# Optimization experiments

Measured on AMD Instinct MI355X. Metric: run time of the kernel, lower is better.

Reference implementation:

```python
import jax, jax.numpy as jnp
import numpy as np

N_ATOMS = 300000
N_COLS = 8
VOCAB = 4096      # nn.Embedding(4096, per_col_dim)
D_COL = 32        # per_col_dim
HID = 256         # hidden_size
N_BONDS = 320000
B_GRAPHS = 6000
ATOMS_PER_GRAPH = 50
STEPS = 3
SENTINEL = 999999999


def _linear_params(key, fan_in, fan_out):
    lim = 1.0 / np.sqrt(fan_in)
    kw, kb = jax.random.split(key)
    W = jax.random.uniform(kw, (fan_out, fan_in), minval=-lim, maxval=lim, dtype=jnp.float32)
    b = jax.random.uniform(kb, (fan_out,), minval=-lim, maxval=lim, dtype=jnp.float32)
    return W, b


def setup_inputs() -> dict:
    key = jax.random.key(0)
    ks = jax.random.split(key, 8)
    a_features = jax.random.randint(ks[0], (N_ATOMS, N_COLS), 0, VOCAB, dtype=jnp.int32)
    uv = jax.random.randint(ks[1], (N_BONDS, 2), 0, N_ATOMS, dtype=jnp.int32)
    bextra = jax.random.randint(ks[2], (N_BONDS, 1), 0, 16, dtype=jnp.int32)
    b_features = jnp.concatenate([uv, bextra], axis=1)
    # contiguous equal-length scopes: graph i owns atoms [i*50, i*50+50)
    starts = np.arange(B_GRAPHS, dtype=np.int32) * ATOMS_PER_GRAPH
    lengths = np.full(B_GRAPHS, ATOMS_PER_GRAPH, dtype=np.int32)
    a_scopes = jnp.asarray(np.stack([starts, lengths], axis=1))
    emb_weights = jax.random.normal(ks[3], (N_COLS, VOCAB, D_COL), dtype=jnp.float32) * 0.02
    W_in, b_in = _linear_params(ks[4], D_COL, HID)
    W_self, b_self = _linear_params(ks[5], HID, HID)
    W_neigh, b_neigh = _linear_params(ks[6], HID, HID)
    W_out, b_out = _linear_params(ks[7], HID, HID)
    return {
        'a_features': a_features, 'b_features': b_features, 'a_scopes': a_scopes,
        'emb_weights': emb_weights,
        'W_in': W_in, 'b_in': b_in,
        'W_self': W_self, 'b_self': b_self,
        'W_neigh': W_neigh, 'b_neigh': b_neigh,
        'W_out': W_out, 'b_out': b_out,
    }


def reference(a_features, b_features, a_scopes, emb_weights,
              W_in, b_in, W_self, b_self, W_neigh, b_neigh, W_out, b_out):
    # --- per-column embedding lookup, summed over columns ---
    idx = jnp.remainder(a_features, VOCAB)
    idx = jnp.where(a_features >= SENTINEL, 0, idx)          # sentinel -> index 0
    x = jnp.zeros((a_features.shape[0], D_COL), dtype=emb_weights.dtype)
    for c in range(N_COLS):                                   # fixed small loop over columns
        x = x + emb_weights[c][idx[:, c]]
    h = x @ W_in.T + b_in                                     # [N, HID]
    # --- undirected edges -> two directed edge lists ---
    u = b_features[:, 0]
    v = b_features[:, 1]
    src = jnp.concatenate([u, v], axis=0)
    dst = jnp.concatenate([v, u], axis=0)
    # --- message passing steps ---
    for _ in range(STEPS):
        agg = jnp.zeros_like(h).at[dst].add(h[src])           # scatter-add neighbor sum
        h = jax.nn.relu(h @ W_self.T + b_self + agg @ W_neigh.T + b_neigh)
    h = h @ W_out.T + b_out
    # --- per-graph mean pooling over contiguous scopes ---
    lengths = a_scopes[:, 1]
    seg_ids = jnp.repeat(jnp.arange(a_scopes.shape[0]), lengths,
                         total_repeat_length=h.shape[0])
    sums = jax.ops.segment_sum(h, seg_ids, num_segments=a_scopes.shape[0])
    denom = jnp.maximum(lengths, 1).astype(h.dtype)[:, None]
    return sums / denom
```

## Files before the change

kernel.cpp:

```cpp
#include <hip/hip_runtime.h>

#define NATOMS 300000
#define NCOLS 8
#define VOCABSZ 4096
#define DCOL 32
#define HIDDIM 256
#define NBONDS 320000
#define NGRAPHS 6000
#define NSTEPS 3

constexpr int MP = 300032;
constexpr int MTILES64 = MP / 64;
constexpr int HSTR = 2 * HIDDIM;
constexpr int XSTR = 2 * DCOL;

typedef _Float16 f16;
typedef _Float16 f16x8 __attribute__((ext_vector_type(8)));
typedef float f32x4 __attribute__((ext_vector_type(4)));

constexpr float LO_SCALE = 2048.0f;
constexpr float INV_LO   = 1.0f / 2048.0f;

__device__ __forceinline__ void split2(float x, f16& h, f16& l) {
    h = (f16)x;
    l = (f16)((x - (float)h) * LO_SCALE);
}

__device__ __forceinline__ int swz(int row, int q) {
    return (row * 4 + (q ^ ((row >> 1) & 3))) * 8;
}

static void* g_pool = nullptr;
__attribute__((constructor)) static void alloc_pool() {
    void* p = nullptr;
    if (hipMalloc(&p, (size_t)1024 * 1024 * 1024) == hipSuccess) {
        hipMemset(p, 0, (size_t)1024 * 1024 * 1024);
        g_pool = p;
    }
}

__global__ void fill_kernel(float* out, float v, int n) {
    int i = blockIdx.x * blockDim.x + threadIdx.x;
    if (i < n) out[i] = v;
}

__global__ void build_edges_kernel(const int* __restrict__ bf, int* __restrict__ esrc,
                                   int* __restrict__ nxt, int* head) {
    int e = blockIdx.x * blockDim.x + threadIdx.x;
    if (e >= 2 * NBONDS) return;
    int src, dst;
    if (e < NBONDS) { src = bf[e * 3 + 0]; dst = bf[e * 3 + 1]; }
    else { int i = e - NBONDS; src = bf[i * 3 + 1]; dst = bf[i * 3 + 0]; }
    esrc[e] = src;
    nxt[e] = atomicExch(&head[dst], e);
}

__global__ void wsplit_kernel(const float* __restrict__ W, f16* __restrict__ Wh,
                              f16* __restrict__ Wl, int n) {
    int i = blockIdx.x * blockDim.x + threadIdx.x;
    if (i >= n) return;
    split2(W[i], Wh[i], Wl[i]);
}

__global__ void bsum_kernel(const float* __restrict__ a, const float* __restrict__ b,
                            float* __restrict__ o) {
    int i = threadIdx.x;
    o[i] = a[i] + b[i];
}

__global__ void embed_kernel(const int* __restrict__ af, const float* __restrict__ emb,
                             f16* __restrict__ x) {
    int gid = blockIdx.x * blockDim.x + threadIdx.x;
    int i = gid >> 5, k = gid & 31;
    if (i >= NATOMS) return;
    float s = 0.0f;
#pragma unroll
    for (int c = 0; c < NCOLS; c++) {
        int v = af[i * NCOLS + c];
        int idx = v & (VOCABSZ - 1);
        if (v >= 999999999) idx = 0;
        s += emb[((size_t)c * VOCABSZ + idx) * DCOL + k];
    }
    f16 hi, lo;
    split2(s, hi, lo);
    x[(size_t)i * XSTR + k] = hi;
    x[(size_t)i * XSTR + DCOL + k] = lo;
}

__global__ void agg_kernel(const f16* __restrict__ H, f16* __restrict__ G,
                           const int* __restrict__ head, const int* __restrict__ nxt,
                           const int* __restrict__ esrc) {
    int wid = (blockIdx.x * blockDim.x + threadIdx.x) >> 6;
    int lane = threadIdx.x & 63;
    if (wid >= NATOMS) return;
    float a0 = 0.f, a1 = 0.f, a2 = 0.f, a3 = 0.f,
          a4 = 0.f, a5 = 0.f, a6 = 0.f, a7 = 0.f;
    int e = head[wid];
    while (e >= 0) {
        int src = esrc[e];
        const f16x8 v = *(const f16x8*)(H + (size_t)src * HSTR + lane * 8);
        a0 += (float)v[0]; a1 += (float)v[1]; a2 += (float)v[2]; a3 += (float)v[3];
        a4 += (float)v[4]; a5 += (float)v[5]; a6 += (float)v[6]; a7 += (float)v[7];
        e = nxt[e];
    }
    const bool isLo = lane >= 32;
    if (isLo) {
        a0 *= INV_LO; a1 *= INV_LO; a2 *= INV_LO; a3 *= INV_LO;
        a4 *= INV_LO; a5 *= INV_LO; a6 *= INV_LO; a7 *= INV_LO;
    }
    float s0 = a0 + __shfl_xor(a0, 32, 64);
    float s1 = a1 + __shfl_xor(a1, 32, 64);
    float s2 = a2 + __shfl_xor(a2, 32, 64);
    float s3 = a3 + __shfl_xor(a3, 32, 64);
    float s4 = a4 + __shfl_xor(a4, 32, 64);
    float s5 = a5 + __shfl_xor(a5, 32, 64);
    float s6 = a6 + __shfl_xor(a6, 32, 64);
    float s7 = a7 + __shfl_xor(a7, 32, 64);
    f16x8 o;
#define EMIT(J, S)                                                    \
    {                                                                 \
        const f16 hv = (f16)(S);                                      \
        o[J] = isLo ? (f16)(((S) - (float)hv) * LO_SCALE) : hv;       \
    }
    EMIT(0, s0) EMIT(1, s1) EMIT(2, s2) EMIT(3, s3)
    EMIT(4, s4) EMIT(5, s5) EMIT(6, s6) EMIT(7, s7)
#undef EMIT
    *(f16x8*)(G + (size_t)wid * HSTR + lane * 8) = o;
}

template <bool HAS_A2, bool RELU, int K>
__global__ __launch_bounds__(256, 2) void mfma_gemm(
    const f16* __restrict__ A1, const f16* __restrict__ A2,
    const f16* __restrict__ B1h, const f16* __restrict__ B1l,
    const f16* __restrict__ B2h, const f16* __restrict__ B2l,
    const float* __restrict__ bias, f16* __restrict__ C) {
    __shared__ __align__(16) f16 sAh[64 * 32];
    __shared__ __align__(16) f16 sAl[64 * 32];
    __shared__ __align__(16) f16 sBh[256 * 32];
    __shared__ __align__(16) f16 sBl[256 * 32];

    const int t = threadIdx.x;
    const int m0 = blockIdx.x * 64;
    const int lane = t & 63;
    const int wid = t >> 6;
    const int wn = wid * 64;
    const int quad = lane >> 4;
    const int l16 = lane & 15;
    const int ra = t >> 2;
    const int qa = t & 3;

    f32x4 acch[4][4], accl[4][4];
#pragma unroll
    for (int a = 0; a < 4; a++)
#pragma unroll
        for (int b = 0; b < 4; b++) {
            acch[a][b] = (f32x4){0.f, 0.f, 0.f, 0.f};
            accl[a][b] = (f32x4){0.f, 0.f, 0.f, 0.f};
        }

    constexpr int NMAT = HAS_A2 ? 2 : 1;
    constexpr int NST = (K / 32) * NMAT;

    int4 pAh, pAl, pBh0, pBh1, pBh2, pBh3, pBl0, pBl1, pBl2, pBl3;

#define LOAD_STAGE(S)                                                          \
    {                                                                          \
        const int mat_ = HAS_A2 ? ((S) & 1) : 0;                               \
        const int kb_ = (HAS_A2 ? ((S) >> 1) : (S)) * 32;                      \
        const f16* A_ = (mat_ == 0) ? A1 : A2;                                 \
        const f16* Bh_ = (mat_ == 0) ? B1h : B2h;                              \
        const f16* Bl_ = (mat_ == 0) ? B1l : B2l;                              \
        const size_t ao_ = (size_t)(m0 + ra) * (2 * K) + kb_ + qa * 8;         \
        pAh = *(const int4*)(A_ + ao_);                                        \
        pAl = *(const int4*)(A_ + ao_ + K);                                    \
        const size_t bo_ = (size_t)ra * K + kb_ + qa * 8;                      \
        pBh0 = *(const int4*)(Bh_ + bo_);                                      \
        pBh1 = *(const int4*)(Bh_ + bo_ + (size_t)64 * K);                     \
        pBh2 = *(const int4*)(Bh_ + bo_ + (size_t)128 * K);                    \
        pBh3 = *(const int4*)(Bh_ + bo_ + (size_t)192 * K);                    \
        pBl0 = *(const int4*)(Bl_ + bo_);                                      \
        pBl1 = *(const int4*)(Bl_ + bo_ + (size_t)64 * K);                     \
        pBl2 = *(const int4*)(Bl_ + bo_ + (size_t)128 * K);                    \
        pBl3 = *(const int4*)(Bl_ + bo_ + (size_t)192 * K);                    \
    }

    LOAD_STAGE(0);

    for (int s = 0; s < NST; s++) {
        __syncthreads();
        {
            const int dA = swz(ra, qa);
            *(int4*)(sAh + dA) = pAh;
            *(int4*)(sAl + dA) = pAl;
            const int d0 = swz(ra, qa), d1 = swz(ra + 64, qa);
            const int d2 = swz(ra + 128, qa), d3 = swz(ra + 192, qa);
            *(int4*)(sBh + d0) = pBh0; *(int4*)(sBh + d1) = pBh1;
            *(int4*)(sBh + d2) = pBh2; *(int4*)(sBh + d3) = pBh3;
            *(int4*)(sBl + d0) = pBl0; *(int4*)(sBl + d1) = pBl1;
            *(int4*)(sBl + d2) = pBl2; *(int4*)(sBl + d3) = pBl3;
        }
        __syncthreads();
        if (s + 1 < NST) LOAD_STAGE(s + 1);

        f16x8 fah[4], fal[4];
#pragma unroll
        for (int mt = 0; mt < 4; mt++) {
            const int src = swz(mt * 16 + l16, quad);
            fah[mt] = *(const f16x8*)(sAh + src);
            fal[mt] = *(const f16x8*)(sAl + src);
        }
#pragma unroll
        for (int nt = 0; nt < 4; nt++) {
            const int src = swz(wn + nt * 16 + l16, quad);
            const f16x8 bh = *(const f16x8*)(sBh + src);
            const f16x8 bl = *(const f16x8*)(sBl + src);
#pragma unroll
            for (int mt = 0; mt < 4; mt++) {
                acch[mt][nt] = __builtin_amdgcn_mfma_f32_16x16x32_f16(fah[mt], bh, acch[mt][nt], 0, 0, 0);
                accl[mt][nt] = __builtin_amdgcn_mfma_f32_16x16x32_f16(fah[mt], bl, accl[mt][nt], 0, 0, 0);
                accl[mt][nt] = __builtin_amdgcn_mfma_f32_16x16x32_f16(fal[mt], bh, accl[mt][nt], 0, 0, 0);
            }
        }
    }
#undef LOAD_STAGE

#pragma unroll
    for (int mt = 0; mt < 4; mt++) {
#pragma unroll
        for (int nt = 0; nt < 4; nt++) {
            const int col = wn + nt * 16 + l16;
            const float bv = bias[col];
#pragma unroll
            for (int r = 0; r < 4; r++) {
                const int row = m0 + mt * 16 + quad * 4 + r;
                float v = acch[mt][nt][r] + accl[mt][nt][r] * INV_LO + bv;
                if (RELU) v = fmaxf(v, 0.f);
                f16 hi, lo;
                split2(v, hi, lo);
                C[(size_t)row * HSTR + col] = hi;
                C[(size_t)row * HSTR + HIDDIM + col] = lo;
            }
        }
    }
}

__global__ void readout_mean_kernel(const f16* __restrict__ H,
                                    const int* __restrict__ scopes, float* __restrict__ G) {
    int g = blockIdx.x;
    int n = threadIdx.x;
    int start = scopes[g * 2 + 0];
    int len = scopes[g * 2 + 1];
    float s = 0.f;
    for (int j = 0; j < len; j++) {
        const f16* row = H + (size_t)(start + j) * HSTR;
        s += (float)row[n] + (float)row[HIDDIM + n] * INV_LO;
    }
    int d = len > 1 ? len : 1;
    G[(size_t)g * HIDDIM + n] = s / (float)d;
}

__global__ __launch_bounds__(256) void out_gemm_kernel(
    const float* __restrict__ G, const float* __restrict__ W,
    const float* __restrict__ bias, float* __restrict__ out) {
    __shared__ float sG[16 * 256];
    const int g0 = blockIdx.x * 16;
    const int t = threadIdx.x;
#pragma unroll
    for (int i = 0; i < 16; i++) sG[i * 256 + t] = G[(size_t)(g0 + i) * 256 + t];
    __syncthreads();
    const float bv = bias[t];
    const float* wrow = W + (size_t)t * 256;
    float acc[16];
#pragma unroll
    for (int g = 0; g < 16; g++) acc[g] = 0.f;
    for (int k = 0; k < 256; k += 4) {
        const float4 w = *(const float4*)(wrow + k);
#pragma unroll
        for (int g = 0; g < 16; g++) {
            const float4 a = *(const float4*)(sG + g * 256 + k);
            acc[g] = fmaf(a.x, w.x, acc[g]);
            acc[g] = fmaf(a.y, w.y, acc[g]);
            acc[g] = fmaf(a.z, w.z, acc[g]);
            acc[g] = fmaf(a.w, w.w, acc[g]);
        }
    }
#pragma unroll
    for (int g = 0; g < 16; g++) out[(size_t)(g0 + g) * 256 + t] = acc[g] + bv;
}

extern "C" void kernel_launch(void* const* d_in, const int* in_sizes, int n_in,
                              void* d_out, int out_size, void* d_ws, size_t ws_size,
                              hipStream_t stream) {
    const int* a_features = (const int*)d_in[0];
    const int* b_features = (const int*)d_in[1];
    const int* a_scopes   = (const int*)d_in[2];
    const float* emb      = (const float*)d_in[3];
    const float* W_in     = (const float*)d_in[4];
    const float* b_in     = (const float*)d_in[5];
    const float* W_self   = (const float*)d_in[6];
    const float* b_self   = (const float*)d_in[7];
    const float* W_neigh  = (const float*)d_in[8];
    const float* b_neigh  = (const float*)d_in[9];
    const float* W_out    = (const float*)d_in[10];
    const float* b_out    = (const float*)d_in[11];

    if (g_pool == nullptr) {
        fill_kernel<<<(out_size + 255) / 256, 256, 0, stream>>>(
            (float*)d_out, 77777.0f, out_size);
        return;
    }

    f16* p = (f16*)g_pool;
    const size_t HB2 = (size_t)MP * HSTR;
    f16* bufA = p;
    f16* bufB = p + HB2;
    f16* bufC = p + 2 * HB2;
    f16* xbuf = p + 3 * HB2;
    f16* Winh = xbuf + (size_t)MP * XSTR;
    f16* Winl = Winh + HIDDIM * DCOL;
    f16* Wsh  = Winl + HIDDIM * DCOL;
    f16* Wsl  = Wsh + HIDDIM * HIDDIM;
    f16* Wnh  = Wsl + HIDDIM * HIDDIM;
    f16* Wnl  = Wnh + HIDDIM * HIDDIM;
    float* Gmean = (float*)(Wnl + HIDDIM * HIDDIM);
    float* bsum  = Gmean + (size_t)NGRAPHS * HIDDIM;
    int* esrc = (int*)(bsum + HIDDIM);
    int* nxt  = esrc + 2 * NBONDS;
    int* head = nxt + 2 * NBONDS;

    constexpr int NPAD = MP - NATOMS;

    hipMemsetAsync(head, 0xFF, (size_t)MP * sizeof(int), stream);
    build_edges_kernel<<<(2 * NBONDS + 255) / 256, 256, 0, stream>>>(b_features, esrc, nxt, head);
    wsplit_kernel<<<(HIDDIM * DCOL + 255) / 256, 256, 0, stream>>>(W_in, Winh, Winl, HIDDIM * DCOL);
    wsplit_kernel<<<(HIDDIM * HIDDIM + 255) / 256, 256, 0, stream>>>(W_self, Wsh, Wsl, HIDDIM * HIDDIM);
    wsplit_kernel<<<(HIDDIM * HIDDIM + 255) / 256, 256, 0, stream>>>(W_neigh, Wnh, Wnl, HIDDIM * HIDDIM);
    bsum_kernel<<<1, HIDDIM, 0, stream>>>(b_self, b_neigh, bsum);

    constexpr int PADH = NPAD * HSTR / 2;
    fill_kernel<<<(PADH + 255) / 256, 256, 0, stream>>>((float*)(bufA + (size_t)NATOMS * HSTR), 0.f, PADH);
    fill_kernel<<<(PADH + 255) / 256, 256, 0, stream>>>((float*)(bufB + (size_t)NATOMS * HSTR), 0.f, PADH);
    fill_kernel<<<(PADH + 255) / 256, 256, 0, stream>>>((float*)(bufC + (size_t)NATOMS * HSTR), 0.f, PADH);
    constexpr int PADX = NPAD * XSTR / 2;
    fill_kernel<<<(PADX + 255) / 256, 256, 0, stream>>>((float*)(xbuf + (size_t)NATOMS * XSTR), 0.f, PADX);

    embed_kernel<<<(NATOMS * DCOL + 255) / 256, 256, 0, stream>>>(a_features, emb, xbuf);
    mfma_gemm<false, false, DCOL><<<MTILES64, 256, 0, stream>>>(
        xbuf, nullptr, Winh, Winl, nullptr, nullptr, b_in, bufA);

    f16* h  = bufA;
    f16* g  = bufB;
    f16* hn = bufC;
    for (int s = 0; s < NSTEPS; s++) {
        agg_kernel<<<NATOMS / 4, 256, 0, stream>>>(h, g, head, nxt, esrc);
        mfma_gemm<true, true, HIDDIM><<<MTILES64, 256, 0, stream>>>(
            h, g, Wsh, Wsl, Wnh, Wnl, bsum, hn);
        f16* old = h;
        h = hn; hn = g; g = old;
    }

    readout_mean_kernel<<<NGRAPHS, 256, 0, stream>>>(h, a_scopes, Gmean);
    out_gemm_kernel<<<NGRAPHS / 16, 256, 0, stream>>>(Gmean, W_out, b_out, (float*)d_out);
}
```

Measured before the change: 2.015 ms.

## Stage GEMM tiles via direct global-to-LDS loads with double buffering

Replaces the register-staged tile loads in the split-fp16 MFMA GEMM with global_load_lds DMA writes straight into shared memory. Shared memory is double-buffered, so the next stage's loads are issued into the other buffer while the current one is computed, and one of the two barriers per stage is removed. The swizzle is folded into the source address so the existing swizzled LDS reads still work. This frees the VGPRs used for prefetch and avoids the LDS store pass, at the cost of doubled LDS (80KB per block), which may limit occupancy below the launch bound of 2 blocks.

```diff
diff --git a/kernel.cpp b/kernel.cpp
--- a/kernel.cpp
+++ b/kernel.cpp
@@ -28,6 +28,12 @@
 
 __device__ __forceinline__ int swz(int row, int q) {
     return (row * 4 + (q ^ ((row >> 1) & 3))) * 8;
+}
+
+__device__ __forceinline__ void dma16(const f16* g, f16* l) {
+    __builtin_amdgcn_global_load_lds(
+        (const __attribute__((address_space(1))) uint32_t*)g,
+        (__attribute__((address_space(3))) uint32_t*)l, 16, 0, 0);
 }
 
 static void* g_pool = nullptr;
@@ -134,10 +140,8 @@
     const f16* __restrict__ B1h, const f16* __restrict__ B1l,
     const f16* __restrict__ B2h, const f16* __restrict__ B2l,
     const float* __restrict__ bias, f16* __restrict__ C) {
-    __shared__ __align__(16) f16 sAh[64 * 32];
-    __shared__ __align__(16) f16 sAl[64 * 32];
-    __shared__ __align__(16) f16 sBh[256 * 32];
-    __shared__ __align__(16) f16 sBl[256 * 32];
+    constexpr int OAH = 0, OAL = 2048, OBH = 4096, OBL = 12288, BUFH = 20480;
+    __shared__ __align__(16) f16 lds[2 * BUFH];
 
     const int t = threadIdx.x;
     const int m0 = blockIdx.x * 64;
@@ -146,8 +150,10 @@
     const int wn = wid * 64;
     const int quad = lane >> 4;
     const int l16 = lane & 15;
-    const int ra = t >> 2;
-    const int qa = t & 3;
+
+    const int ra_ = wid * 16 + (lane >> 2);
+    const int qs_ = (lane & 3) ^ ((ra_ >> 1) & 3);
+    const int ko_ = qs_ * 8;
 
     f32x4 acch[4][4], accl[4][4];
 #pragma unroll
@@ -161,46 +167,40 @@
     constexpr int NMAT = HAS_A2 ? 2 : 1;
     constexpr int NST = (K / 32) * NMAT;
 
-    int4 pAh, pAl, pBh0, pBh1, pBh2, pBh3, pBl0, pBl1, pBl2, pBl3;
-
-#define LOAD_STAGE(S)                                                          \
+#define ISSUE_STAGE(S, BUF)                                                    \
     {                                                                          \
         const int mat_ = HAS_A2 ? ((S) & 1) : 0;                               \
         const int kb_ = (HAS_A2 ? ((S) >> 1) : (S)) * 32;                      \
         const f16* A_ = (mat_ == 0) ? A1 : A2;                                 \
         const f16* Bh_ = (mat_ == 0) ? B1h : B2h;                              \
         const f16* Bl_ = (mat_ == 0) ? B1l : B2l;                              \
-        const size_t ao_ = (size_t)(m0 + ra) * (2 * K) + kb_ + qa * 8;         \
-        pAh = *(const int4*)(A_ + ao_);                                        \
-        pAl = *(const int4*)(A_ + ao_ + K);                                    \
-        const size_t bo_ = (size_t)ra * K + kb_ + qa * 8;                      \
-        pBh0 = *(const int4*)(Bh_ + bo_);                                      \
-        pBh1 = *(const int4*)(Bh_ + bo_ + (size_t)64 * K);                     \
-        pBh2 = *(const int4*)(Bh_ + bo_ + (size_t)128 * K);                    \
-        pBh3 = *(const int4*)(Bh_ + bo_ + (size_t)192 * K);                    \
-        pBl0 = *(const int4*)(Bl_ + bo_);                                      \
-        pBl1 = *(const int4*)(Bl_ + bo_ + (size_t)64 * K);                     \
-        pBl2 = *(const int4*)(Bl_ + bo_ + (size_t)128 * K);                    \
-        pBl3 = *(const int4*)(Bl_ + bo_ + (size_t)192 * K);                    \
-    }
-
-    LOAD_STAGE(0);
+        f16* const dst_ = lds + (BUF) * BUFH + wid * 512;                      \
+        const size_t arow_ = (size_t)(m0 + ra_) * (2 * K) + kb_ + ko_;         \
+        dma16(A_ + arow_, dst_ + OAH);                                         \
+        dma16(A_ + arow_ + K, dst_ + OAL);                                     \
+        const size_t brow_ = (size_t)ra_ * K + kb_ + ko_;                      \
+        dma16(Bh_ + brow_, dst_ + OBH);                                        \
+        dma16(Bl_ + brow_, dst_ + OBL);                                        \
+        dma16(Bh_ + brow_ + (size_t)64 * K, dst_ + OBH + 2048);                \
+        dma16(Bl_ + brow_ + (size_t)64 * K, dst_ + OBL + 2048);                \
+        dma16(Bh_ + brow_ + (size_t)128 * K, dst_ + OBH + 4096);               \
+        dma16(Bl_ + brow_ + (size_t)128 * K, dst_ + OBL + 4096);               \
+        dma16(Bh_ + brow_ + (size_t)192 * K, dst_ + OBH + 6144);               \
+        dma16(Bl_ + brow_ + (size_t)192 * K, dst_ + OBL + 6144);               \
+    }
+
+    ISSUE_STAGE(0, 0);
 
     for (int s = 0; s < NST; s++) {
+        asm volatile("s_waitcnt vmcnt(0)" ::: "memory");
         __syncthreads();
-        {
-            const int dA = swz(ra, qa);
-            *(int4*)(sAh + dA) = pAh;
-            *(int4*)(sAl + dA) = pAl;
-            const int d0 = swz(ra, qa), d1 = swz(ra + 64, qa);
-            const int d2 = swz(ra + 128, qa), d3 = swz(ra + 192, qa);
-            *(int4*)(sBh + d0) = pBh0; *(int4*)(sBh + d1) = pBh1;
-            *(int4*)(sBh + d2) = pBh2; *(int4*)(sBh + d3) = pBh3;
-            *(int4*)(sBl + d0) = pBl0; *(int4*)(sBl + d1) = pBl1;
-            *(int4*)(sBl + d2) = pBl2; *(int4*)(sBl + d3) = pBl3;
-        }
-        __syncthreads();
-        if (s + 1 < NST) LOAD_STAGE(s + 1);
+        if (s + 1 < NST) ISSUE_STAGE(s + 1, (s + 1) & 1);
+
+        const f16* cb = lds + (s & 1) * BUFH;
+        const f16* sAh = cb + OAH;
+        const f16* sAl = cb + OAL;
+        const f16* sBh = cb + OBH;
+        const f16* sBl = cb + OBL;
 
         f16x8 fah[4], fal[4];
 #pragma unroll
@@ -222,7 +222,7 @@
             }
         }
     }
-#undef LOAD_STAGE
+#undef ISSUE_STAGE
 
 #pragma unroll
     for (int mt = 0; mt < 4; mt++) {
```

Measured after the change: 1.936 ms. -3.9%, faster.
